# Kernel optimization log

Hardware: AMD Instinct MI355X
Metric: run time of the kernel (lower is better)

Reference implementation:

```python
import jax, jax.numpy as jnp
import numpy as np

EMBED_DIM = 768
NUM_HEADS = 12
D_K = EMBED_DIM // NUM_HEADS


def setup_inputs() -> dict:
    key = jax.random.key(0)
    ks = jax.random.split(key, 9)
    b, s, d = 4, 2048, EMBED_DIM
    scale = 1.0 / np.sqrt(d)
    x = jax.random.normal(ks[0], (b, s, d), dtype=jnp.float32)
    return {
        "x": x,
        "w_q": jax.random.normal(ks[1], (d, d), dtype=jnp.float32) * scale,
        "b_q": jnp.zeros((d,), dtype=jnp.float32),
        "w_k": jax.random.normal(ks[2], (d, d), dtype=jnp.float32) * scale,
        "b_k": jnp.zeros((d,), dtype=jnp.float32),
        "w_v": jax.random.normal(ks[3], (d, d), dtype=jnp.float32) * scale,
        "b_v": jnp.zeros((d,), dtype=jnp.float32),
        "w_o": jax.random.normal(ks[4], (d, d), dtype=jnp.float32) * scale,
        "b_o": jnp.zeros((d,), dtype=jnp.float32),
    }


def reference(x, w_q, b_q, w_k, b_k, w_v, b_v, w_o, b_o):
    b, s, d = x.shape
    h, dk = NUM_HEADS, D_K
    # projections (torch Linear: x @ W^T + b)
    q = (x @ w_q.T + b_q).reshape(b, s, h, dk).transpose(0, 2, 1, 3)
    k = (x @ w_k.T + b_k).reshape(b, s, h, dk).transpose(0, 2, 1, 3)
    v = (x @ w_v.T + b_v).reshape(b, s, h, dk).transpose(0, 2, 1, 3)
    # causal attention: full [b,h,s,s] scores as in the original
    scores = jnp.einsum("bhqd,bhkd->bhqk", q, k) / jnp.sqrt(jnp.float32(dk))
    causal = jnp.tril(jnp.ones((s, s), dtype=bool))
    scores = jnp.where(causal[None, None], scores, -jnp.inf)
    attn = jax.nn.softmax(scores, axis=-1)
    out = jnp.einsum("bhqk,bhkd->bhqd", attn, v)
    out = out.transpose(0, 2, 1, 3).reshape(b, s, h * dk)
    return out @ w_o.T + b_o
```

## Files before the change

kernel.cpp:

```cpp
#include <hip/hip_runtime.h>
#include <hip/hip_bf16.h>
#include <stdint.h>

typedef short bf16x8 __attribute__((ext_vector_type(8)));
typedef float f32x4 __attribute__((ext_vector_type(4)));
typedef unsigned short u16;


__device__ __forceinline__ u16 f2bf_bits(float f) {
    __hip_bfloat16 h = __float2bfloat16(f);
    return __builtin_bit_cast(u16, h);
}

__device__ __forceinline__ uint32_t pack2bf(float a, float b) {
    uint32_t ua = __builtin_bit_cast(uint32_t, a) + 0x8000u;
    uint32_t ub = __builtin_bit_cast(uint32_t, b) + 0x8000u;
    return __builtin_amdgcn_perm(ub, ua, 0x07060302u);
}

__device__ __forceinline__ void gld_lds16(const void* g, void* l) {
    __builtin_amdgcn_global_load_lds(
        (const __attribute__((address_space(1))) void*)g,
        (__attribute__((address_space(3))) void*)l, 16, 0, 0);
}

#define CEXP 0.18033688011112042f


__global__ __launch_bounds__(256) void cast_all_kernel(
    const float* __restrict__ x, const float* __restrict__ w0,
    const float* __restrict__ w1, const float* __restrict__ w2,
    const float* __restrict__ w3, u16* __restrict__ xb,
    u16* __restrict__ o0, u16* __restrict__ o1,
    u16* __restrict__ o2, u16* __restrict__ o3,
    const float* __restrict__ bq, const float* __restrict__ bk,
    const float* __restrict__ bv, float* __restrict__ biasf) {
    int gid = blockIdx.x * 256 + threadIdx.x;
    const float* s;
    u16* d;
    int off;
    float mul = 1.0f;
    if (gid < 1572864) {
        s = x; d = xb; off = gid;
    } else {
        int g2 = gid - 1572864;
        int which = g2 / 147456;
        off = g2 - which * 147456;
        s = which == 0 ? w0 : which == 1 ? w1 : which == 2 ? w2 : w3;
        d = which == 0 ? o0 : which == 1 ? o1 : which == 2 ? o2 : o3;
        if (which == 0) mul = CEXP;
    }
    float4 v = ((const float4*)s)[off];
    ushort4 u;
    u.x = f2bf_bits(v.x * mul); u.y = f2bf_bits(v.y * mul);
    u.z = f2bf_bits(v.z * mul); u.w = f2bf_bits(v.w * mul);
    ((ushort4*)d)[off] = u;
    if (gid < 2304) {
        float bb = gid < 768 ? bq[gid] * CEXP
                             : gid < 1536 ? bk[gid - 768] : bv[gid - 1536];
        biasf[gid] = bb;
    }
}


template <int RT, int MODE, int MINW>
__global__ __launch_bounds__(256, MINW) void gemm_xwt(
    const u16* __restrict__ X, const u16* __restrict__ W,
    const float* __restrict__ bias, float* __restrict__ Cf,
    u16* __restrict__ Cb, u16* __restrict__ Vt, int K, int NC) {
    constexpr int JR = RT / 32;
    constexpr int XSZ = RT * 64;
    constexpr int WSZ = 128 * 64;
    __shared__ u16 pool[2 * XSZ + 2 * WSZ];
    const int tid = threadIdx.x;
    const int w = tid >> 6, lane = tid & 63;
    const int quad = lane >> 4, l15 = lane & 15;
    const int m0 = blockIdx.y * RT, n0 = blockIdx.x * 128;
    const int wr = (w >> 1) * (RT / 2), wc = (w & 1) * 64;
    const int rr = lane >> 3, c8 = lane & 7;

    auto stage = [&](int kt, int pb) {
        const int k0 = kt * 64;
        u16* bx = pool + pb * XSZ;
        u16* bw = pool + 2 * XSZ + pb * WSZ;
        for (int cb = w; cb < RT / 8; cb += 4) {
            int row = cb * 8 + rr;
            int cg = c8 ^ ((rr ^ cb) & 7);
            gld_lds16(X + (size_t)(m0 + row) * K + k0 + cg * 8, &bx[cb * 512]);
        }
        for (int cb = w; cb < 16; cb += 4) {
            int row = cb * 8 + rr;
            int cg = c8 ^ ((rr ^ cb) & 7);
            gld_lds16(W + (size_t)(n0 + row) * K + k0 + cg * 8, &bw[cb * 512]);
        }
    };

    f32x4 acc[JR][4];
    for (int j = 0; j < JR; ++j)
        for (int i = 0; i < 4; ++i) acc[j][i] = (f32x4){0.f, 0.f, 0.f, 0.f};

    const int KT = K / 64;
    stage(0, 0);
    __syncthreads();
    for (int kt = 0; kt < KT; ++kt) {
        const int pb = kt & 1;
        if (kt + 1 < KT) stage(kt + 1, pb ^ 1);
        const u16* bx = pool + pb * XSZ;
        const u16* bw = pool + 2 * XSZ + pb * WSZ;
        for (int kk = 0; kk < 2; ++kk) {
            bf16x8 xf[JR], wf[4];
            for (int j = 0; j < JR; ++j) {
                int row = wr + j * 16 + l15;
                int slot = (kk * 4 + quad) ^ ((row ^ (row >> 3)) & 7);
                xf[j] = *(const bf16x8*)&bx[row * 64 + slot * 8];
            }
            for (int i = 0; i < 4; ++i) {
                int row = wc + i * 16 + l15;
                int slot = (kk * 4 + quad) ^ ((row ^ (row >> 3)) & 7);
                wf[i] = *(const bf16x8*)&bw[row * 64 + slot * 8];
            }
            for (int j = 0; j < JR; ++j)
                for (int i = 0; i < 4; ++i)
                    acc[j][i] = __builtin_amdgcn_mfma_f32_16x16x32_bf16(
                        wf[i], xf[j], acc[j][i], 0, 0, 0);
        }
        __syncthreads();
    }

    const bool vtile = (MODE == 2) && (n0 >= 1536);
    if (vtile) {
        u16* T2 = pool;
        for (int i = 0; i < 4; ++i) {
            int nl = wc + i * 16 + quad * 4;
            int c0 = n0 + nl;
            float4 bv4 = *(const float4*)&bias[c0];
            for (int j = 0; j < JR; ++j) {
                int ml = wr + j * 16 + l15;
                T2[(nl + 0) * 136 + ml] = f2bf_bits(acc[j][i][0] + bv4.x);
                T2[(nl + 1) * 136 + ml] = f2bf_bits(acc[j][i][1] + bv4.y);
                T2[(nl + 2) * 136 + ml] = f2bf_bits(acc[j][i][2] + bv4.z);
                T2[(nl + 3) * 136 + ml] = f2bf_bits(acc[j][i][3] + bv4.w);
            }
        }
        __syncthreads();
        int sc = (tid & 15) * 8;
        int bq_ = m0 >> 11;
        int s0 = m0 & 2047;
        for (int rnd = 0; rnd < 8; ++rnd) {
            int dl = (tid >> 4) + rnd * 16;
            bf16x8 vv = *(const bf16x8*)&T2[dl * 136 + sc];
            int dg = n0 + dl - 1536;
            int h = dg >> 6, dd = dg & 63;
            *(bf16x8*)&Vt[((size_t)(bq_ * 12 + h) * 64 + dd) * 2048 + s0 + sc] = vv;
        }
    } else {
        for (int i = 0; i < 4; ++i) {
            int c0 = n0 + wc + i * 16 + quad * 4;
            float4 bv4 = *(const float4*)&bias[c0];
            for (int j = 0; j < JR; ++j) {
                int row = m0 + wr + j * 16 + l15;
                float v0 = acc[j][i][0] + bv4.x;
                float v1 = acc[j][i][1] + bv4.y;
                float v2 = acc[j][i][2] + bv4.z;
                float v3 = acc[j][i][3] + bv4.w;
                if (MODE == 1) {
                    float4 o4 = {v0, v1, v2, v3};
                    *(float4*)&Cf[(size_t)row * NC + c0] = o4;
                } else {
                    uint2 pk = {pack2bf(v0, v1), pack2bf(v2, v3)};
                    *(uint2*)&Cb[(size_t)row * NC + c0] = pk;
                }
            }
        }
    }
}


__global__ __launch_bounds__(256, 3) void attn_kernel(
    const u16* __restrict__ QKV, const u16* __restrict__ Vt, u16* __restrict__ O) {
    __shared__ u16 lsKV[2 * 128 * 64];
    __shared__ u16 lsP[4][32 * 72];

    int bx = blockIdx.x;
    int bh = bx % 48;
    int qtb = 15 - (bx / 48);
    int b = bh / 12, h = bh % 12;
    int tid = threadIdx.x, w = tid >> 6, lane = tid & 63;
    int quad = lane >> 4, l15 = lane & 15;
    int rr = lane >> 3, c8 = lane & 7;

    auto stageKV = [&](int kt, int pb) {
        u16* dst = lsKV + pb * 8192;
        for (int cb = w; cb < 16; cb += 4) {
            int r = (cb & 7) * 8 + rr;
            int cg = c8 ^ ((rr ^ cb) & 7);
            const u16* g = (cb < 8)
                ? QKV + (size_t)(b * 2048 + kt * 64 + r) * 2304 + 768 + h * 64 + cg * 8
                : Vt + (size_t)(bh * 64 + r) * 2048 + kt * 64 + cg * 8;
            gld_lds16(g, &dst[cb * 512]);
        }
    };

    {
        u16* qs = lsKV + 8192;
        for (int cb = w; cb < 16; cb += 4) {
            int row = cb * 8 + rr;
            int cg = c8 ^ ((rr ^ cb) & 7);
            gld_lds16(QKV + (size_t)(b * 2048 + qtb * 128 + row) * 2304 + h * 64 + cg * 8,
                      &qs[cb * 512]);
        }
    }
    stageKV(0, 0);
    __syncthreads();

    bf16x8 q0[2], q1[2];
    for (int g = 0; g < 2; ++g) {
        const u16* qs = lsKV + 8192;
        int rowq = g * 64 + w * 16 + l15;
        int swq = (rowq ^ (rowq >> 3)) & 7;
        q0[g] = *(const bf16x8*)&qs[rowq * 64 + ((0 + quad) ^ swq) * 8];
        q1[g] = *(const bf16x8*)&qs[rowq * 64 + ((4 + quad) ^ swq) * 8];
    }
    __syncthreads();

    const bf16x8 ones = {(short)0x3F80, (short)0x3F80, (short)0x3F80, (short)0x3F80,
                         (short)0x3F80, (short)0x3F80, (short)0x3F80, (short)0x3F80};
    f32x4 oacc0[4], oacc1[4], lacc0, lacc1;
    for (int dt = 0; dt < 4; ++dt) {
        oacc0[dt] = (f32x4){0.f, 0.f, 0.f, 0.f};
        oacc1[dt] = (f32x4){0.f, 0.f, 0.f, 0.f};
    }
    lacc0 = (f32x4){0.f, 0.f, 0.f, 0.f};
    lacc1 = (f32x4){0.f, 0.f, 0.f, 0.f};
    u16* Pw = lsP[w];
    const int qrel = w * 16 + l15;
    const int ktmax = 2 * qtb + 1;

    for (int kt = 0; kt <= ktmax; ++kt) {
        const int pb = kt & 1;
        if (kt < ktmax) stageKV(kt + 1, pb ^ 1);
        const u16* Kf = lsKV + pb * 8192;
        const u16* Vf = Kf + 4096;
        const bool do0 = (kt <= 2 * qtb);

        f32x4 S0[4], S1[4];
        for (int ct = 0; ct < 4; ++ct) {
            int rowk = ct * 16 + l15;
            int swk = (rowk ^ (rowk >> 3)) & 7;
            bf16x8 k0 = *(const bf16x8*)&Kf[rowk * 64 + ((0 + quad) ^ swk) * 8];
            bf16x8 k1 = *(const bf16x8*)&Kf[rowk * 64 + ((4 + quad) ^ swk) * 8];
            f32x4 z = (f32x4){0.f, 0.f, 0.f, 0.f};
            S1[ct] = __builtin_amdgcn_mfma_f32_16x16x32_bf16(k0, q0[1], z, 0, 0, 0);
            S1[ct] = __builtin_amdgcn_mfma_f32_16x16x32_bf16(k1, q1[1], S1[ct], 0, 0, 0);
            if (do0) {
                S0[ct] = __builtin_amdgcn_mfma_f32_16x16x32_bf16(k0, q0[0], z, 0, 0, 0);
                S0[ct] = __builtin_amdgcn_mfma_f32_16x16x32_bf16(k1, q1[0], S0[ct], 0, 0, 0);
            }
        }

        if (kt == 2 * qtb) {
            for (int ct = 0; ct < 4; ++ct) {
                int kbase = ct * 16 + quad * 4;
                for (int r = 0; r < 4; ++r)
                    if (kbase + r > qrel) S0[ct][r] = -1e30f;
            }
        }
        if (kt == 2 * qtb + 1) {
            for (int ct = 0; ct < 4; ++ct) {
                int kbase = ct * 16 + quad * 4;
                for (int r = 0; r < 4; ++r)
                    if (kbase + r > qrel) S1[ct][r] = -1e30f;
            }
        }

        if (do0) {
            u16* Pr = &Pw[(size_t)l15 * 72];
            for (int ct = 0; ct < 4; ++ct) {
                float p0 = __builtin_amdgcn_exp2f(S0[ct][0]);
                float p1 = __builtin_amdgcn_exp2f(S0[ct][1]);
                float p2 = __builtin_amdgcn_exp2f(S0[ct][2]);
                float p3 = __builtin_amdgcn_exp2f(S0[ct][3]);
                uint2 pk = {pack2bf(p0, p1), pack2bf(p2, p3)};
                *(uint2*)&Pr[ct * 16 + quad * 4] = pk;
            }
        }
        {
            u16* Pr = &Pw[(size_t)(16 + l15) * 72];
            for (int ct = 0; ct < 4; ++ct) {
                float p0 = __builtin_amdgcn_exp2f(S1[ct][0]);
                float p1 = __builtin_amdgcn_exp2f(S1[ct][1]);
                float p2 = __builtin_amdgcn_exp2f(S1[ct][2]);
                float p3 = __builtin_amdgcn_exp2f(S1[ct][3]);
                uint2 pk = {pack2bf(p0, p1), pack2bf(p2, p3)};
                *(uint2*)&Pr[ct * 16 + quad * 4] = pk;
            }
        }

        for (int ks = 0; ks < 2; ++ks) {
            bf16x8 bp1 = *(const bf16x8*)&Pw[(size_t)(16 + l15) * 72 + ks * 32 + quad * 8];
            bf16x8 bp0;
            if (do0) bp0 = *(const bf16x8*)&Pw[(size_t)l15 * 72 + ks * 32 + quad * 8];
            lacc1 = __builtin_amdgcn_mfma_f32_16x16x32_bf16(ones, bp1, lacc1, 0, 0, 0);
            if (do0)
                lacc0 = __builtin_amdgcn_mfma_f32_16x16x32_bf16(ones, bp0, lacc0, 0, 0, 0);
            for (int dt = 0; dt < 4; ++dt) {
                int rowv = dt * 16 + l15;
                int swv = (rowv ^ (rowv >> 3)) & 7;
                bf16x8 av = *(const bf16x8*)&Vf[rowv * 64 + ((ks * 4 + quad) ^ swv) * 8];
                oacc1[dt] = __builtin_amdgcn_mfma_f32_16x16x32_bf16(av, bp1, oacc1[dt], 0, 0, 0);
                if (do0)
                    oacc0[dt] = __builtin_amdgcn_mfma_f32_16x16x32_bf16(av, bp0, oacc0[dt], 0, 0, 0);
            }
        }
        __syncthreads();
    }

    float inv0 = 1.0f / lacc0[0], inv1 = 1.0f / lacc1[0];
    for (int g = 0; g < 2; ++g) {
        float inv = g ? inv1 : inv0;
        f32x4* oa = g ? oacc1 : oacc0;
        int row = qtb * 128 + g * 64 + w * 16 + l15;
        for (int dt = 0; dt < 4; ++dt) {
            uint2 pk = {pack2bf(oa[dt][0] * inv, oa[dt][1] * inv),
                        pack2bf(oa[dt][2] * inv, oa[dt][3] * inv)};
            *(uint2*)&O[(size_t)(b * 2048 + row) * 768 + h * 64 + dt * 16 + quad * 4] = pk;
        }
    }
}


extern "C" void kernel_launch(void* const* d_in, const int* in_sizes, int n_in,
                              void* d_out, int out_size, void* d_ws, size_t ws_size,
                              hipStream_t stream) {
    const float* x  = (const float*)d_in[0];
    const float* wq = (const float*)d_in[1];
    const float* bq = (const float*)d_in[2];
    const float* wk = (const float*)d_in[3];
    const float* bk = (const float*)d_in[4];
    const float* wv = (const float*)d_in[5];
    const float* bv = (const float*)d_in[6];
    const float* wo = (const float*)d_in[7];
    const float* bo = (const float*)d_in[8];
    float* out = (float*)d_out;

    char* ws = (char*)d_ws;
    u16*   xb    = (u16*)(ws + 0);
    u16*   Wf    = (u16*)(ws + 12582912);
    u16*   wob   = (u16*)(ws + 16121856);
    float* biasf = (float*)(ws + 17301504);
    u16*   QKVb  = (u16*)(ws + 17310720);
    u16*   Vtw   = (u16*)(ws + 55059456);
    u16*   Ow    = (u16*)(ws + 67642368);

    cast_all_kernel<<<8448, 256, 0, stream>>>(x, wq, wk, wv, wo,
                                              xb, Wf, Wf + 589824, Wf + 1179648, wob,
                                              bq, bk, bv, biasf);

    gemm_xwt<128, 2, 2><<<dim3(18, 64), 256, 0, stream>>>(xb, Wf, biasf, nullptr,
                                                          QKVb, Vtw, 768, 2304);
    attn_kernel<<<768, 256, 0, stream>>>(QKVb, Vtw, Ow);
    gemm_xwt<64, 1, 3><<<dim3(6, 128), 256, 0, stream>>>(Ow, wob, bo, out, nullptr,
                                                         nullptr, 768, 768);
}
```

Measured before the change: 221.1 us.

## Drop LDS double buffering for occupancy and pair query tiles for causal balance

Both GEMMs and the attention kernel switch from double-buffered LDS staging to single-buffered loads with a barrier before and after each tile. This roughly halves shared memory use, and the launch bounds are raised to target more resident blocks per CU. The attention kernel now gives each block a pair of 64-row query tiles (j and 31-j) instead of one contiguous 128-row tile, so causal work is balanced evenly across blocks. The cost is that global-to-LDS loads are no longer overlapped with compute inside a block, so latency hiding depends on other resident waves.

```diff
diff --git a/kernel.cpp b/kernel.cpp
--- a/kernel.cpp
+++ b/kernel.cpp
@@ -70,8 +70,9 @@
     u16* __restrict__ Cb, u16* __restrict__ Vt, int K, int NC) {
     constexpr int JR = RT / 32;
     constexpr int XSZ = RT * 64;
-    constexpr int WSZ = 128 * 64;
-    __shared__ u16 pool[2 * XSZ + 2 * WSZ];
+    constexpr int BSZ = XSZ + 128 * 64;
+    constexpr int PSZ = (MODE == 2 && BSZ < 128 * 136) ? 128 * 136 : BSZ;
+    __shared__ u16 pool[PSZ];
     const int tid = threadIdx.x;
     const int w = tid >> 6, lane = tid & 63;
     const int quad = lane >> 4, l15 = lane & 15;
@@ -79,56 +80,48 @@
     const int wr = (w >> 1) * (RT / 2), wc = (w & 1) * 64;
     const int rr = lane >> 3, c8 = lane & 7;
 
-    auto stage = [&](int kt, int pb) {
+    f32x4 acc[JR][4];
+    for (int j = 0; j < JR; ++j)
+        for (int i = 0; i < 4; ++i) acc[j][i] = (f32x4){0.f, 0.f, 0.f, 0.f};
+
+    const int KT = K / 64;
+    for (int kt = 0; kt < KT; ++kt) {
         const int k0 = kt * 64;
-        u16* bx = pool + pb * XSZ;
-        u16* bw = pool + 2 * XSZ + pb * WSZ;
+        __syncthreads();
         for (int cb = w; cb < RT / 8; cb += 4) {
             int row = cb * 8 + rr;
             int cg = c8 ^ ((rr ^ cb) & 7);
-            gld_lds16(X + (size_t)(m0 + row) * K + k0 + cg * 8, &bx[cb * 512]);
+            gld_lds16(X + (size_t)(m0 + row) * K + k0 + cg * 8, &pool[cb * 512]);
         }
         for (int cb = w; cb < 16; cb += 4) {
             int row = cb * 8 + rr;
             int cg = c8 ^ ((rr ^ cb) & 7);
-            gld_lds16(W + (size_t)(n0 + row) * K + k0 + cg * 8, &bw[cb * 512]);
-        }
-    };
-
-    f32x4 acc[JR][4];
-    for (int j = 0; j < JR; ++j)
-        for (int i = 0; i < 4; ++i) acc[j][i] = (f32x4){0.f, 0.f, 0.f, 0.f};
-
-    const int KT = K / 64;
-    stage(0, 0);
-    __syncthreads();
-    for (int kt = 0; kt < KT; ++kt) {
-        const int pb = kt & 1;
-        if (kt + 1 < KT) stage(kt + 1, pb ^ 1);
-        const u16* bx = pool + pb * XSZ;
-        const u16* bw = pool + 2 * XSZ + pb * WSZ;
+            gld_lds16(W + (size_t)(n0 + row) * K + k0 + cg * 8, &pool[XSZ + cb * 512]);
+        }
+        __syncthreads();
+
         for (int kk = 0; kk < 2; ++kk) {
             bf16x8 xf[JR], wf[4];
             for (int j = 0; j < JR; ++j) {
                 int row = wr + j * 16 + l15;
                 int slot = (kk * 4 + quad) ^ ((row ^ (row >> 3)) & 7);
-                xf[j] = *(const bf16x8*)&bx[row * 64 + slot * 8];
+                xf[j] = *(const bf16x8*)&pool[row * 64 + slot * 8];
             }
             for (int i = 0; i < 4; ++i) {
                 int row = wc + i * 16 + l15;
                 int slot = (kk * 4 + quad) ^ ((row ^ (row >> 3)) & 7);
-                wf[i] = *(const bf16x8*)&bw[row * 64 + slot * 8];
+                wf[i] = *(const bf16x8*)&pool[XSZ + row * 64 + slot * 8];
             }
             for (int j = 0; j < JR; ++j)
                 for (int i = 0; i < 4; ++i)
                     acc[j][i] = __builtin_amdgcn_mfma_f32_16x16x32_bf16(
                         wf[i], xf[j], acc[j][i], 0, 0, 0);
         }
-        __syncthreads();
     }
 
     const bool vtile = (MODE == 2) && (n0 >= 1536);
     if (vtile) {
+        __syncthreads();
         u16* T2 = pool;
         for (int i = 0; i < 4; ++i) {
             int nl = wc + i * 16 + quad * 4;
@@ -176,79 +169,69 @@
 }
 
 
-__global__ __launch_bounds__(256, 3) void attn_kernel(
+__global__ __launch_bounds__(256, 4) void attn_kernel(
     const u16* __restrict__ QKV, const u16* __restrict__ Vt, u16* __restrict__ O) {
-    __shared__ u16 lsKV[2 * 128 * 64];
+    __shared__ u16 kv[8192];
     __shared__ u16 lsP[4][32 * 72];
 
     int bx = blockIdx.x;
     int bh = bx % 48;
-    int qtb = 15 - (bx / 48);
+    int j = bx / 48;
+    int jj = 31 - j;
     int b = bh / 12, h = bh % 12;
     int tid = threadIdx.x, w = tid >> 6, lane = tid & 63;
     int quad = lane >> 4, l15 = lane & 15;
     int rr = lane >> 3, c8 = lane & 7;
 
-    auto stageKV = [&](int kt, int pb) {
-        u16* dst = lsKV + pb * 8192;
+    for (int cb = w; cb < 16; cb += 4) {
+        int row = (cb & 7) * 8 + rr;
+        int qrow = (cb < 8 ? j * 64 : jj * 64) + row;
+        int cg = c8 ^ ((rr ^ cb) & 7);
+        gld_lds16(QKV + (size_t)(b * 2048 + qrow) * 2304 + h * 64 + cg * 8,
+                  &kv[cb * 512]);
+    }
+    __syncthreads();
+
+    bf16x8 q0[2], q1[2];
+    for (int g = 0; g < 2; ++g) {
+        int rowq = g * 64 + w * 16 + l15;
+        int swq = (rowq ^ (rowq >> 3)) & 7;
+        q0[g] = *(const bf16x8*)&kv[rowq * 64 + ((0 + quad) ^ swq) * 8];
+        q1[g] = *(const bf16x8*)&kv[rowq * 64 + ((4 + quad) ^ swq) * 8];
+    }
+
+    const bf16x8 ones = {(short)0x3F80, (short)0x3F80, (short)0x3F80, (short)0x3F80,
+                         (short)0x3F80, (short)0x3F80, (short)0x3F80, (short)0x3F80};
+    f32x4 oacc0[4], oacc1[4], lacc0, lacc1;
+    for (int dt = 0; dt < 4; ++dt) {
+        oacc0[dt] = (f32x4){0.f, 0.f, 0.f, 0.f};
+        oacc1[dt] = (f32x4){0.f, 0.f, 0.f, 0.f};
+    }
+    lacc0 = (f32x4){0.f, 0.f, 0.f, 0.f};
+    lacc1 = (f32x4){0.f, 0.f, 0.f, 0.f};
+    u16* Pw = lsP[w];
+    const int qrel = w * 16 + l15;
+
+    for (int kt = 0; kt <= jj; ++kt) {
+        __syncthreads();
         for (int cb = w; cb < 16; cb += 4) {
             int r = (cb & 7) * 8 + rr;
             int cg = c8 ^ ((rr ^ cb) & 7);
             const u16* g = (cb < 8)
                 ? QKV + (size_t)(b * 2048 + kt * 64 + r) * 2304 + 768 + h * 64 + cg * 8
                 : Vt + (size_t)(bh * 64 + r) * 2048 + kt * 64 + cg * 8;
-            gld_lds16(g, &dst[cb * 512]);
-        }
-    };
-
-    {
-        u16* qs = lsKV + 8192;
-        for (int cb = w; cb < 16; cb += 4) {
-            int row = cb * 8 + rr;
-            int cg = c8 ^ ((rr ^ cb) & 7);
-            gld_lds16(QKV + (size_t)(b * 2048 + qtb * 128 + row) * 2304 + h * 64 + cg * 8,
-                      &qs[cb * 512]);
-        }
-    }
-    stageKV(0, 0);
-    __syncthreads();
-
-    bf16x8 q0[2], q1[2];
-    for (int g = 0; g < 2; ++g) {
-        const u16* qs = lsKV + 8192;
-        int rowq = g * 64 + w * 16 + l15;
-        int swq = (rowq ^ (rowq >> 3)) & 7;
-        q0[g] = *(const bf16x8*)&qs[rowq * 64 + ((0 + quad) ^ swq) * 8];
-        q1[g] = *(const bf16x8*)&qs[rowq * 64 + ((4 + quad) ^ swq) * 8];
-    }
-    __syncthreads();
-
-    const bf16x8 ones = {(short)0x3F80, (short)0x3F80, (short)0x3F80, (short)0x3F80,
-                         (short)0x3F80, (short)0x3F80, (short)0x3F80, (short)0x3F80};
-    f32x4 oacc0[4], oacc1[4], lacc0, lacc1;
-    for (int dt = 0; dt < 4; ++dt) {
-        oacc0[dt] = (f32x4){0.f, 0.f, 0.f, 0.f};
-        oacc1[dt] = (f32x4){0.f, 0.f, 0.f, 0.f};
-    }
-    lacc0 = (f32x4){0.f, 0.f, 0.f, 0.f};
-    lacc1 = (f32x4){0.f, 0.f, 0.f, 0.f};
-    u16* Pw = lsP[w];
-    const int qrel = w * 16 + l15;
-    const int ktmax = 2 * qtb + 1;
-
-    for (int kt = 0; kt <= ktmax; ++kt) {
-        const int pb = kt & 1;
-        if (kt < ktmax) stageKV(kt + 1, pb ^ 1);
-        const u16* Kf = lsKV + pb * 8192;
-        const u16* Vf = Kf + 4096;
-        const bool do0 = (kt <= 2 * qtb);
+            gld_lds16(g, &kv[cb * 512]);
+        }
+        __syncthreads();
+
+        const bool do0 = (kt <= j);
 
         f32x4 S0[4], S1[4];
         for (int ct = 0; ct < 4; ++ct) {
             int rowk = ct * 16 + l15;
             int swk = (rowk ^ (rowk >> 3)) & 7;
-            bf16x8 k0 = *(const bf16x8*)&Kf[rowk * 64 + ((0 + quad) ^ swk) * 8];
-            bf16x8 k1 = *(const bf16x8*)&Kf[rowk * 64 + ((4 + quad) ^ swk) * 8];
+            bf16x8 k0 = *(const bf16x8*)&kv[rowk * 64 + ((0 + quad) ^ swk) * 8];
+            bf16x8 k1 = *(const bf16x8*)&kv[rowk * 64 + ((4 + quad) ^ swk) * 8];
             f32x4 z = (f32x4){0.f, 0.f, 0.f, 0.f};
             S1[ct] = __builtin_amdgcn_mfma_f32_16x16x32_bf16(k0, q0[1], z, 0, 0, 0);
             S1[ct] = __builtin_amdgcn_mfma_f32_16x16x32_bf16(k1, q1[1], S1[ct], 0, 0, 0);
@@ -258,14 +241,14 @@
             }
         }
 
-        if (kt == 2 * qtb) {
+        if (kt == j) {
             for (int ct = 0; ct < 4; ++ct) {
                 int kbase = ct * 16 + quad * 4;
                 for (int r = 0; r < 4; ++r)
                     if (kbase + r > qrel) S0[ct][r] = -1e30f;
             }
         }
-        if (kt == 2 * qtb + 1) {
+        if (kt == jj) {
             for (int ct = 0; ct < 4; ++ct) {
                 int kbase = ct * 16 + quad * 4;
                 for (int r = 0; r < 4; ++r)
@@ -306,20 +289,19 @@
             for (int dt = 0; dt < 4; ++dt) {
                 int rowv = dt * 16 + l15;
                 int swv = (rowv ^ (rowv >> 3)) & 7;
-                bf16x8 av = *(const bf16x8*)&Vf[rowv * 64 + ((ks * 4 + quad) ^ swv) * 8];
+                bf16x8 av = *(const bf16x8*)&kv[4096 + rowv * 64 + ((ks * 4 + quad) ^ swv) * 8];
                 oacc1[dt] = __builtin_amdgcn_mfma_f32_16x16x32_bf16(av, bp1, oacc1[dt], 0, 0, 0);
                 if (do0)
                     oacc0[dt] = __builtin_amdgcn_mfma_f32_16x16x32_bf16(av, bp0, oacc0[dt], 0, 0, 0);
             }
         }
-        __syncthreads();
     }
 
     float inv0 = 1.0f / lacc0[0], inv1 = 1.0f / lacc1[0];
     for (int g = 0; g < 2; ++g) {
         float inv = g ? inv1 : inv0;
         f32x4* oa = g ? oacc1 : oacc0;
-        int row = qtb * 128 + g * 64 + w * 16 + l15;
+        int row = (g ? jj : j) * 64 + w * 16 + l15;
         for (int dt = 0; dt < 4; ++dt) {
             uint2 pk = {pack2bf(oa[dt][0] * inv, oa[dt][1] * inv),
                         pack2bf(oa[dt][2] * inv, oa[dt][3] * inv)};
@@ -356,9 +338,9 @@
                                               xb, Wf, Wf + 589824, Wf + 1179648, wob,
                                               bq, bk, bv, biasf);
 
-    gemm_xwt<128, 2, 2><<<dim3(18, 64), 256, 0, stream>>>(xb, Wf, biasf, nullptr,
+    gemm_xwt<128, 2, 4><<<dim3(18, 64), 256, 0, stream>>>(xb, Wf, biasf, nullptr,
                                                           QKVb, Vtw, 768, 2304);
     attn_kernel<<<768, 256, 0, stream>>>(QKVb, Vtw, Ow);
-    gemm_xwt<64, 1, 3><<<dim3(6, 128), 256, 0, stream>>>(Ow, wob, bo, out, nullptr,
+    gemm_xwt<64, 1, 4><<<dim3(6, 128), 256, 0, stream>>>(Ow, wob, bo, out, nullptr,
                                                          nullptr, 768, 768);
 }
```

New measurement: 231.8 us. 1.05x slower.
